# Kernel optimization log

Measured on AMD Instinct MI355X. Metric: run time of the kernel, lower is better.

The kernel has to match this reference:

```python
import jax, jax.numpy as jnp
import numpy as np


def setup_inputs() -> dict:
    key = jax.random.key(0)
    k1, k2, k3, k4, k5 = jax.random.split(key, 5)
    B, S, H, L = 32, 4096, 512, 2
    scale = 1.0 / np.sqrt(H)
    return {
        "out": jax.random.normal(k1, (B, S, H), dtype=jnp.float32),
        "hidden": jax.random.normal(k2, (L, B, H), dtype=jnp.float32),
        "W": jax.random.normal(k3, (H, H), dtype=jnp.float32) * scale,
        "b": jax.random.normal(k4, (H,), dtype=jnp.float32) * scale,
        "v": jax.random.normal(k5, (H,), dtype=jnp.float32) * scale,
    }


def reference(out, hidden, W, b, v):
    # hidden_last: (B, 1, H) from last layer
    h_last = hidden[-1][:, None, :]
    # energy = tanh(out @ W^T + b + h_last)  -> (B, S, H)
    energy = jnp.tanh(jnp.einsum("bsh,oh->bso", out, W) + b + h_last)
    # scores = energy @ v  -> (B, S)
    scores = jnp.einsum("bsh,h->bs", energy, v)
    attn = jax.nn.softmax(scores, axis=-1)
    # context = sum_s attn[b,s] * out[b,s,:]  -> (B, H)
    context = jnp.einsum("bs,bsh->bh", attn, out)
    return (context, attn)
```

## Files before the change

kernel.cpp:

```cpp
#include <hip/hip_runtime.h>
#include <hip/hip_bf16.h>

#define B_ 32
#define S_ 4096
#define H_ 512
#define M_ (B_ * S_)
#define L_ 2

typedef __bf16 bf16;
typedef bf16 bf16x8 __attribute__((ext_vector_type(8)));
typedef float floatx4 __attribute__((ext_vector_type(4)));
typedef float floatx16 __attribute__((ext_vector_type(16)));

__device__ inline bf16 f2b(float f) { return (bf16)f; }

__device__ inline float fast_tanh(float x) {
    float xc = fminf(15.0f, fmaxf(-15.0f, x));
    float e = __expf(2.0f * xc);
    return (e - 1.0f) * __builtin_amdgcn_rcpf(e + 1.0f);
}

__global__ __launch_bounds__(256) void convert_Wfrag(const float* __restrict__ W,
                                                     bf16* __restrict__ Wf) {
    int gid  = blockIdx.x * 256 + threadIdx.x;
    int lane = gid & 63;
    int ks   = (gid >> 6) & 31;
    int nt   = gid >> 11;
    int row  = nt * 32 + (lane & 31);
    int col  = ks * 16 + (lane >> 5) * 8;
    const float* src = W + (size_t)row * H_ + col;
    floatx4 f0 = *(const floatx4*)src;
    floatx4 f1 = *(const floatx4*)(src + 4);
    bf16x8 p = { f2b(f0[0]), f2b(f0[1]), f2b(f0[2]), f2b(f0[3]),
                 f2b(f1[0]), f2b(f1[1]), f2b(f1[2]), f2b(f1[3]) };
    *(bf16x8*)(Wf + (size_t)gid * 8) = p;
}

#define MT 64

__global__ __launch_bounds__(256, 2) void scores_kernel(
    const float* __restrict__ outT,
    const bf16*  __restrict__ Wf,
    const float* __restrict__ bias,
    const float* __restrict__ hidden,
    const float* __restrict__ v,
    float* __restrict__ scores,
    float* __restrict__ pc,
    float* __restrict__ lmaxg,
    float* __restrict__ lsumg)
{
    __shared__ bf16 Alds[MT * 512];

    const int tid  = threadIdx.x;
    const int wave = tid >> 6;
    const int lane = tid & 63;
    const int l31  = lane & 31;
    const int half = lane >> 5;

    const int m0    = blockIdx.x * MT;
    const int batch = m0 >> 12;

    {
        const floatx4* src = (const floatx4*)(outT + (size_t)m0 * H_);
        #pragma unroll 4
        for (int it = 0; it < 16; ++it) {
            int idx = it * 256 + tid;
            int r   = idx >> 6;
            int j   = idx & 63;
            floatx4 f0 = __builtin_nontemporal_load(src + idx * 2);
            floatx4 f1 = __builtin_nontemporal_load(src + idx * 2 + 1);
            bf16x8 p = { f2b(f0[0]), f2b(f0[1]), f2b(f0[2]), f2b(f0[3]),
                         f2b(f1[0]), f2b(f1[1]), f2b(f1[2]), f2b(f1[3]) };
            int frag = (r >> 5) * 32 + (j >> 1);
            int slot = (j & 1) * 32 + ((r + (j >> 1)) & 31);
            *(bf16x8*)&Alds[frag * 512 + slot * 8] = p;
        }
    }
    __syncthreads();

    const bf16* wf = Wf + (size_t)(wave * 4) * 32 * 512 + lane * 8;

    floatx16 acc[2][4];
    #pragma unroll
    for (int mt = 0; mt < 2; ++mt)
        #pragma unroll
        for (int nt = 0; nt < 4; ++nt)
            acc[mt][nt] = (floatx16)(0.0f);

    bf16x8 bb[4][4];
    bf16x8 aa[2][2];
    #pragma unroll
    for (int p = 0; p < 4; ++p)
        #pragma unroll
        for (int nt = 0; nt < 4; ++nt)
            bb[p][nt] = *(const bf16x8*)(wf + nt * 16384 + p * 512);
    #pragma unroll
    for (int mt = 0; mt < 2; ++mt)
        aa[0][mt] = *(const bf16x8*)
            &Alds[(mt * 32 + 0) * 512 + (half * 32 + (l31 & 31)) * 8];

    #pragma unroll
    for (int ks = 0; ks < 32; ++ks) {
        const int cur = ks & 3;
        const int ap  = ks & 1;
        if (ks < 31) {
            const int rot = (l31 + ks + 1) & 31;
            #pragma unroll
            for (int mt = 0; mt < 2; ++mt)
                aa[ap ^ 1][mt] = *(const bf16x8*)
                    &Alds[(mt * 32 + ks + 1) * 512 + (half * 32 + rot) * 8];
        }
        #pragma unroll
        for (int mt = 0; mt < 2; ++mt)
            #pragma unroll
            for (int nt = 0; nt < 4; ++nt)
                acc[mt][nt] = __builtin_amdgcn_mfma_f32_32x32x16_bf16(
                    aa[ap][mt], bb[cur][nt], acc[mt][nt], 0, 0, 0);
        if (ks < 28) {
            #pragma unroll
            for (int nt = 0; nt < 4; ++nt)
                bb[cur][nt] = *(const bf16x8*)(wf + nt * 16384 + (ks + 4) * 512);
        }
    }

    const float* hlast = hidden + (size_t)((L_ - 1) * B_ + batch) * H_;
    float part[2][16];
    #pragma unroll
    for (int mt = 0; mt < 2; ++mt)
        #pragma unroll
        for (int rg = 0; rg < 16; ++rg) part[mt][rg] = 0.0f;

    #pragma unroll
    for (int nt = 0; nt < 4; ++nt) {
        int n = wave * 128 + nt * 32 + l31;
        float bn = bias[n] + hlast[n];
        float vn = v[n];
        #pragma unroll
        for (int mt = 0; mt < 2; ++mt)
            #pragma unroll
            for (int rg = 0; rg < 16; ++rg)
                part[mt][rg] += fast_tanh(acc[mt][nt][rg] + bn) * vn;
    }

    __syncthreads();
    float* sred = (float*)Alds;
    float* pbuf = sred + 256;
    #pragma unroll
    for (int mt = 0; mt < 2; ++mt)
        #pragma unroll
        for (int rg = 0; rg < 16; ++rg) {
            float s = part[mt][rg];
            s += __shfl_xor(s, 1);
            s += __shfl_xor(s, 2);
            s += __shfl_xor(s, 4);
            s += __shfl_xor(s, 8);
            s += __shfl_xor(s, 16);
            if (l31 == 0) {
                int row = (rg & 3) + 8 * (rg >> 2) + 4 * half;
                sred[wave * 64 + mt * 32 + row] = s;
            }
        }
    __syncthreads();

    if (tid < 64) {
        float sc = (sred[tid] + sred[64 + tid]) + (sred[128 + tid] + sred[192 + tid]);
        scores[m0 + tid] = sc;
        float mx = sc;
        #pragma unroll
        for (int off = 32; off >= 1; off >>= 1) mx = fmaxf(mx, __shfl_xor(mx, off));
        float p = __expf(sc - mx);
        pbuf[tid] = p;
        float sm = p;
        #pragma unroll
        for (int off = 32; off >= 1; off >>= 1) sm += __shfl_xor(sm, off);
        if (tid == 0) { lmaxg[blockIdx.x] = mx; lsumg[blockIdx.x] = sm; }
    }
    __syncthreads();

    {
        const float2* op = (const float2*)(outT + (size_t)m0 * H_) + tid;
        float2 a = {0.0f, 0.0f};
        #pragma unroll 8
        for (int s = 0; s < 64; ++s) {
            float2 o = op[s * 256];
            float ps = pbuf[s];
            a.x += ps * o.x;
            a.y += ps * o.y;
        }
        *(float2*)&pc[(size_t)blockIdx.x * H_ + tid * 2] = a;
    }
}

__global__ __launch_bounds__(256) void softmax_kernel(const float* __restrict__ scores,
                                                      float* __restrict__ attn) {
    __shared__ float red[4];
    int b = blockIdx.x, tid = threadIdx.x;
    const float* row = scores + (size_t)b * S_;
    float vals[16];
    float mx = -3.4e38f;
    #pragma unroll
    for (int i = 0; i < 16; ++i) { vals[i] = row[i * 256 + tid]; mx = fmaxf(mx, vals[i]); }
    #pragma unroll
    for (int off = 32; off >= 1; off >>= 1) mx = fmaxf(mx, __shfl_xor(mx, off));
    if ((tid & 63) == 0) red[tid >> 6] = mx;
    __syncthreads();
    mx = fmaxf(fmaxf(red[0], red[1]), fmaxf(red[2], red[3]));
    __syncthreads();
    float sum = 0.f;
    #pragma unroll
    for (int i = 0; i < 16; ++i) { vals[i] = __expf(vals[i] - mx); sum += vals[i]; }
    #pragma unroll
    for (int off = 32; off >= 1; off >>= 1) sum += __shfl_xor(sum, off);
    if ((tid & 63) == 0) red[tid >> 6] = sum;
    __syncthreads();
    float inv = 1.0f / (red[0] + red[1] + red[2] + red[3]);
    #pragma unroll
    for (int i = 0; i < 16; ++i) attn[(size_t)b * S_ + i * 256 + tid] = vals[i] * inv;
}

__global__ __launch_bounds__(256) void context_final(const float* __restrict__ pc,
                                                     const float* __restrict__ lmaxg,
                                                     const float* __restrict__ lsumg,
                                                     float* __restrict__ ctx) {
    __shared__ float e_sh[64];
    __shared__ float inv_sh;
    int b = blockIdx.x, tid = threadIdx.x;
    if (tid < 64) {
        float lm = lmaxg[b * 64 + tid];
        float mx = lm;
        #pragma unroll
        for (int off = 32; off >= 1; off >>= 1) mx = fmaxf(mx, __shfl_xor(mx, off));
        float e = __expf(lm - mx);
        e_sh[tid] = e;
        float gs = e * lsumg[b * 64 + tid];
        #pragma unroll
        for (int off = 32; off >= 1; off >>= 1) gs += __shfl_xor(gs, off);
        if (tid == 0) inv_sh = 1.0f / gs;
    }
    __syncthreads();
    float inv = inv_sh;
    const float2* pp = (const float2*)(pc + (size_t)b * 64 * H_) + tid;
    float2 a = {0.0f, 0.0f};
    #pragma unroll 8
    for (int j = 0; j < 64; ++j) {
        float2 q = pp[j * 256];
        float e = e_sh[j];
        a.x += e * q.x;
        a.y += e * q.y;
    }
    float2 r = { a.x * inv, a.y * inv };
    *(float2*)&ctx[(size_t)b * H_ + tid * 2] = r;
}

extern "C" void kernel_launch(void* const* d_in, const int* in_sizes, int n_in,
                              void* d_out, int out_size, void* d_ws, size_t ws_size,
                              hipStream_t stream) {
    const float* outT   = (const float*)d_in[0];
    const float* hidden = (const float*)d_in[1];
    const float* W      = (const float*)d_in[2];
    const float* bias   = (const float*)d_in[3];
    const float* v      = (const float*)d_in[4];

    float* ctx    = (float*)d_out;
    float* attn   = (float*)d_out + B_ * H_;

    const int NBLK = M_ / MT;
    float* scores = (float*)d_ws;
    bf16*  Wf     = (bf16*)((char*)d_ws + (size_t)M_ * 4);
    float* pc     = (float*)((char*)d_ws + (size_t)M_ * 4 + (size_t)H_ * H_ * 2);
    float* lmaxg  = pc + (size_t)NBLK * H_;
    float* lsumg  = lmaxg + NBLK;

    convert_Wfrag<<<128, 256, 0, stream>>>(W, Wf);
    scores_kernel<<<NBLK, 256, 0, stream>>>(outT, Wf, bias, hidden, v,
                                            scores, pc, lmaxg, lsumg);
    softmax_kernel<<<B_, 256, 0, stream>>>(scores, attn);
    context_final<<<B_, 256, 0, stream>>>(pc, lmaxg, lsumg, ctx);
}
```

Baseline: 485.4 us.

## Split scores kernel N-dimension across 16 waves per 1024-thread block

```diff
diff --git a/kernel.cpp b/kernel.cpp
--- a/kernel.cpp
+++ b/kernel.cpp
@@ -9,6 +9,7 @@
 
 typedef __bf16 bf16;
 typedef bf16 bf16x8 __attribute__((ext_vector_type(8)));
+typedef float floatx2 __attribute__((ext_vector_type(2)));
 typedef float floatx4 __attribute__((ext_vector_type(4)));
 typedef float floatx16 __attribute__((ext_vector_type(16)));
 
@@ -38,7 +39,7 @@
 
 #define MT 64
 
-__global__ __launch_bounds__(256, 2) void scores_kernel(
+__global__ __launch_bounds__(1024, 4) void scores_kernel(
     const float* __restrict__ outT,
     const bf16*  __restrict__ Wf,
     const float* __restrict__ bias,
@@ -60,11 +61,18 @@
     const int m0    = blockIdx.x * MT;
     const int batch = m0 >> 12;
 
+    const bf16* wf = Wf + (size_t)wave * 16384 + lane * 8;
+
+    bf16x8 bb[4];
+    #pragma unroll
+    for (int p = 0; p < 4; ++p)
+        bb[p] = *(const bf16x8*)(wf + p * 512);
+
     {
         const floatx4* src = (const floatx4*)(outT + (size_t)m0 * H_);
-        #pragma unroll 4
-        for (int it = 0; it < 16; ++it) {
-            int idx = it * 256 + tid;
+        #pragma unroll
+        for (int it = 0; it < 4; ++it) {
+            int idx = it * 1024 + tid;
             int r   = idx >> 6;
             int j   = idx & 63;
             floatx4 f0 = __builtin_nontemporal_load(src + idx * 2);
@@ -78,22 +86,11 @@
     }
     __syncthreads();
 
-    const bf16* wf = Wf + (size_t)(wave * 4) * 32 * 512 + lane * 8;
-
-    floatx16 acc[2][4];
-    #pragma unroll
-    for (int mt = 0; mt < 2; ++mt)
-        #pragma unroll
-        for (int nt = 0; nt < 4; ++nt)
-            acc[mt][nt] = (floatx16)(0.0f);
-
-    bf16x8 bb[4][4];
+    floatx16 acc[2];
+    #pragma unroll
+    for (int mt = 0; mt < 2; ++mt) acc[mt] = (floatx16)(0.0f);
+
     bf16x8 aa[2][2];
-    #pragma unroll
-    for (int p = 0; p < 4; ++p)
-        #pragma unroll
-        for (int nt = 0; nt < 4; ++nt)
-            bb[p][nt] = *(const bf16x8*)(wf + nt * 16384 + p * 512);
     #pragma unroll
     for (int mt = 0; mt < 2; ++mt)
         aa[0][mt] = *(const bf16x8*)
@@ -112,44 +109,27 @@
         }
         #pragma unroll
         for (int mt = 0; mt < 2; ++mt)
-            #pragma unroll
-            for (int nt = 0; nt < 4; ++nt)
-                acc[mt][nt] = __builtin_amdgcn_mfma_f32_32x32x16_bf16(
-                    aa[ap][mt], bb[cur][nt], acc[mt][nt], 0, 0, 0);
-        if (ks < 28) {
-            #pragma unroll
-            for (int nt = 0; nt < 4; ++nt)
-                bb[cur][nt] = *(const bf16x8*)(wf + nt * 16384 + (ks + 4) * 512);
-        }
+            acc[mt] = __builtin_amdgcn_mfma_f32_32x32x16_bf16(
+                aa[ap][mt], bb[cur], acc[mt], 0, 0, 0);
+        if (ks < 28)
+            bb[cur] = *(const bf16x8*)(wf + (ks + 4) * 512);
     }
 
     const float* hlast = hidden + (size_t)((L_ - 1) * B_ + batch) * H_;
-    float part[2][16];
+    const int n  = wave * 32 + l31;
+    const float bn = bias[n] + hlast[n];
+    const float vn = v[n];
+
+    __syncthreads();
+    float*   sred  = (float*)Alds;
+    float*   pbuf  = sred + 1024;
+    floatx4* pvred = (floatx4*)(pbuf + 64);
+
     #pragma unroll
     for (int mt = 0; mt < 2; ++mt)
         #pragma unroll
-        for (int rg = 0; rg < 16; ++rg) part[mt][rg] = 0.0f;
-
-    #pragma unroll
-    for (int nt = 0; nt < 4; ++nt) {
-        int n = wave * 128 + nt * 32 + l31;
-        float bn = bias[n] + hlast[n];
-        float vn = v[n];
-        #pragma unroll
-        for (int mt = 0; mt < 2; ++mt)
-            #pragma unroll
-            for (int rg = 0; rg < 16; ++rg)
-                part[mt][rg] += fast_tanh(acc[mt][nt][rg] + bn) * vn;
-    }
-
-    __syncthreads();
-    float* sred = (float*)Alds;
-    float* pbuf = sred + 256;
-    #pragma unroll
-    for (int mt = 0; mt < 2; ++mt)
-        #pragma unroll
         for (int rg = 0; rg < 16; ++rg) {
-            float s = part[mt][rg];
+            float s = fast_tanh(acc[mt][rg] + bn) * vn;
             s += __shfl_xor(s, 1);
             s += __shfl_xor(s, 2);
             s += __shfl_xor(s, 4);
@@ -163,7 +143,9 @@
     __syncthreads();
 
     if (tid < 64) {
-        float sc = (sred[tid] + sred[64 + tid]) + (sred[128 + tid] + sred[192 + tid]);
+        float sc = 0.0f;
+        #pragma unroll
+        for (int w = 0; w < 16; ++w) sc += sred[w * 64 + tid];
         scores[m0 + tid] = sc;
         float mx = sc;
         #pragma unroll
@@ -178,16 +160,21 @@
     __syncthreads();
 
     {
-        const float2* op = (const float2*)(outT + (size_t)m0 * H_) + tid;
-        float2 a = {0.0f, 0.0f};
-        #pragma unroll 8
-        for (int s = 0; s < 64; ++s) {
-            float2 o = op[s * 256];
-            float ps = pbuf[s];
-            a.x += ps * o.x;
-            a.y += ps * o.y;
-        }
-        *(float2*)&pc[(size_t)blockIdx.x * H_ + tid * 2] = a;
+        const int c4 = tid & 127;
+        const int sg = tid >> 7;
+        const floatx4* op = (const floatx4*)(outT + (size_t)(m0 + sg * 8) * H_) + c4;
+        floatx4 a = (floatx4)(0.0f);
+        #pragma unroll
+        for (int j = 0; j < 8; ++j)
+            a += pbuf[sg * 8 + j] * __builtin_nontemporal_load(op + (size_t)j * 128);
+        pvred[sg * 128 + c4] = a;
+    }
+    __syncthreads();
+    if (tid < 128) {
+        floatx4 r = (floatx4)(0.0f);
+        #pragma unroll
+        for (int sg = 0; sg < 8; ++sg) r += pvred[sg * 128 + tid];
+        *(floatx4*)&pc[(size_t)blockIdx.x * H_ + tid * 4] = r;
     }
 }
 
@@ -239,17 +226,15 @@
     }
     __syncthreads();
     float inv = inv_sh;
-    const float2* pp = (const float2*)(pc + (size_t)b * 64 * H_) + tid;
-    float2 a = {0.0f, 0.0f};
+    const floatx2* pp = (const floatx2*)(pc + (size_t)b * 64 * H_) + tid;
+    floatx2 a = (floatx2)(0.0f);
     #pragma unroll 8
     for (int j = 0; j < 64; ++j) {
-        float2 q = pp[j * 256];
-        float e = e_sh[j];
-        a.x += e * q.x;
-        a.y += e * q.y;
-    }
-    float2 r = { a.x * inv, a.y * inv };
-    *(float2*)&ctx[(size_t)b * H_ + tid * 2] = r;
+        floatx2 q = __builtin_nontemporal_load(pp + (size_t)j * 256);
+        a += e_sh[j] * q;
+    }
+    floatx2 r = a * inv;
+    *(floatx2*)&ctx[(size_t)b * H_ + tid * 2] = r;
 }
 
 extern "C" void kernel_launch(void* const* d_in, const int* in_sizes, int n_in,
@@ -272,8 +257,8 @@
     float* lsumg  = lmaxg + NBLK;
 
     convert_Wfrag<<<128, 256, 0, stream>>>(W, Wf);
-    scores_kernel<<<NBLK, 256, 0, stream>>>(outT, Wf, bias, hidden, v,
-                                            scores, pc, lmaxg, lsumg);
+    scores_kernel<<<NBLK, 1024, 0, stream>>>(outT, Wf, bias, hidden, v,
+                                             scores, pc, lmaxg, lsumg);
     softmax_kernel<<<B_, 256, 0, stream>>>(scores, attn);
     context_final<<<B_, 256, 0, stream>>>(pc, lmaxg, lsumg, ctx);
 }
```

Result: slower. 508.9 us (+4.8%).
